# Performance work log

Measured on AMD Instinct MI355X. Metric: run time of the kernel, lower is better.

Reference implementation:

```python
import jax, jax.numpy as jnp
import numpy as np

L = 7
D = 20
V = 2 ** L                      # voxel_size
NUM_EMB = V ** 3
DOM_LO, DOM_HI = -1.0, 1.0
DOM_LEN = DOM_HI - DOM_LO

# 8 corner offsets in the order used by the torch module
OFFSETS = jnp.array([[0, 0, 0], [1, 0, 0], [0, 1, 0], [1, 1, 0],
                     [0, 0, 1], [1, 0, 1], [0, 1, 1], [1, 1, 1]], dtype=jnp.int32)


def setup_inputs() -> dict:
    key = jax.random.key(0)
    kx, kg = jax.random.split(key)
    # points strictly inside the domain so floor()+1 corner stays in-range
    x = jax.random.uniform(kx, (1_000_000, 3), jnp.float32, minval=-1.0, maxval=0.998)
    grid = jax.random.normal(kg, (NUM_EMB, D), jnp.float32) * 0.02  # embedding table
    return {"x": x, "grid": grid}


def reference(x, grid):
    # points -> grid space, floor to lower corner
    gp = jnp.floor((x - DOM_LO) / DOM_LEN * V)                  # [P,3] float
    grid_idx = gp[:, None, :].astype(jnp.int32) + OFFSETS[None]  # [P,8,3]
    # flat index: ix * V^0 + iy * V^1 + iz * V^2
    flat = grid_idx[..., 0] + grid_idx[..., 1] * V + grid_idx[..., 2] * (V * V)
    Q_emb = grid[flat]                                          # [P,8,D] gather
    Q_pos = grid_idx.astype(x.dtype) / V * DOM_LEN + DOM_LO      # [P,8,3] world pos

    px, py, pz = x[:, 0], x[:, 1], x[:, 2]
    x1, x2 = Q_pos[:, 0, 0], Q_pos[:, 1, 0]
    y1, y2 = Q_pos[:, 0, 1], Q_pos[:, 2, 1]
    z1, z2 = Q_pos[:, 0, 2], Q_pos[:, 4, 2]

    q000, q100, q010, q110 = Q_emb[:, 0], Q_emb[:, 1], Q_emb[:, 2], Q_emb[:, 3]
    q001, q101, q011, q111 = Q_emb[:, 4], Q_emb[:, 5], Q_emb[:, 6], Q_emb[:, 7]

    wx0 = ((x2 - px) / (x2 - x1))[:, None]
    wx1 = ((px - x1) / (x2 - x1))[:, None]
    fx0 = wx0 * q000 + wx1 * q100
    fx1 = wx0 * q010 + wx1 * q110
    fx2 = wx0 * q001 + wx1 * q101
    fx3 = wx0 * q011 + wx1 * q111

    wy0 = ((y2 - py) / (y2 - y1))[:, None]
    wy1 = ((py - y1) / (y2 - y1))[:, None]
    fy0 = wy0 * fx0 + wy1 * fx1
    fy1 = wy0 * fx2 + wy1 * fx3

    wz0 = ((z2 - pz) / (z2 - z1))[:, None]
    wz1 = ((pz - z1) / (z2 - z1))[:, None]
    return wz0 * fy0 + wz1 * fy1                                 # [P,D]
```

## Files before the change

### kernel.cpp

```cpp
#include <hip/hip_runtime.h>

#define V 128
#define D 20
#define NUM_EMB (V * V * V)
#define NBUCK 32768
#define BCAP  60
#define OVFCAP 16384
#define REG_ROWS 125
#define REG_CHUNKS 625
#define STAGE_INSTS 10

typedef float v4f __attribute__((ext_vector_type(4)));
typedef unsigned int u32;

typedef const __attribute__((address_space(1))) void gv_t;
typedef __attribute__((address_space(3))) void lv_t;
#define G2L(gsrc, ldst) \
    __builtin_amdgcn_global_load_lds((gv_t*)(gsrc), (lv_t*)(ldst), 16, 0, 0)

__device__ __forceinline__ void compute_chunk(
    const float* __restrict__ x, const float* __restrict__ grid,
    float* __restrict__ out, int i, int k)
{
    float px = x[3 * i + 0];
    float py = x[3 * i + 1];
    float pz = x[3 * i + 2];
    int ix = (int)floorf((px + 1.0f) * 64.0f);
    int iy = (int)floorf((py + 1.0f) * 64.0f);
    int iz = (int)floorf((pz + 1.0f) * 64.0f);

    float x1 = (float)ix * (2.0f / 128.0f) - 1.0f;
    float x2 = (float)(ix + 1) * (2.0f / 128.0f) - 1.0f;
    float y1 = (float)iy * (2.0f / 128.0f) - 1.0f;
    float y2 = (float)(iy + 1) * (2.0f / 128.0f) - 1.0f;
    float z1 = (float)iz * (2.0f / 128.0f) - 1.0f;
    float z2 = (float)(iz + 1) * (2.0f / 128.0f) - 1.0f;

    float wx1 = (px - x1) * 64.0f, wx0 = (x2 - px) * 64.0f;
    float wy1 = (py - y1) * 64.0f, wy0 = (y2 - py) * 64.0f;
    float wz1 = (pz - z1) * 64.0f, wz0 = (z2 - pz) * 64.0f;

    int f000 = ix + iy * V + iz * V * V;
    int flats[8] = { f000,             f000 + 1,
                     f000 + V,         f000 + V + 1,
                     f000 + V * V,     f000 + V * V + 1,
                     f000 + V * V + V, f000 + V * V + V + 1 };
    #pragma unroll
    for (int c = 0; c < 8; c++)
        if (flats[c] > NUM_EMB - 1) flats[c] = NUM_EMB - 1;

    float w[8];
    w[0] = wx0 * wy0 * wz0; w[1] = wx1 * wy0 * wz0;
    w[2] = wx0 * wy1 * wz0; w[3] = wx1 * wy1 * wz0;
    w[4] = wx0 * wy0 * wz1; w[5] = wx1 * wy0 * wz1;
    w[6] = wx0 * wy1 * wz1; w[7] = wx1 * wy1 * wz1;

    v4f q[8];
    #pragma unroll
    for (int c = 0; c < 8; c++)
        q[c] = *(const v4f*)(grid + (size_t)flats[c] * D + 4 * k);

    v4f acc = (v4f)(0.0f);
    #pragma unroll
    for (int c = 0; c < 8; c++) acc += w[c] * q[c];

    __builtin_nontemporal_store(acc, (v4f*)(out + (size_t)i * D + 4 * k));
}

__global__ __launch_bounds__(256) void bin_kernel(
    const float* __restrict__ x, const float* __restrict__ grid,
    float* __restrict__ out, u32* __restrict__ cnt, u32* __restrict__ blist,
    u32* __restrict__ ovfc, u32* __restrict__ ovf, int N)
{
    int i = blockIdx.x * 256 + threadIdx.x;
    if (i >= N) return;
    float px = x[3 * i + 0];
    float py = x[3 * i + 1];
    float pz = x[3 * i + 2];
    int ix = (int)floorf((px + 1.0f) * 64.0f);
    int iy = (int)floorf((py + 1.0f) * 64.0f);
    int iz = (int)floorf((pz + 1.0f) * 64.0f);
    int b = (ix >> 2) + ((iy >> 2) << 5) + ((iz >> 2) << 10);
    u32 pos = atomicAdd(&cnt[b], 1u);
    if (pos < BCAP) {
        blist[(size_t)b * BCAP + pos] = (u32)i;
    } else {
        u32 op = atomicAdd(ovfc, 1u);
        if (op < OVFCAP) ovf[op] = (u32)i;
        else for (int k = 0; k < 5; k++) compute_chunk(x, grid, out, i, k);
    }
}

__global__ __launch_bounds__(128) void gather_kernel(
    const float* __restrict__ x, const float* __restrict__ grid,
    float* __restrict__ out, const u32* __restrict__ cnt,
    const u32* __restrict__ blist)
{
    __shared__ __align__(16) float reg[STAGE_INSTS * 256];

    int bid = blockIdx.x;
    int b = (bid & 7) * (NBUCK / 8) + (bid >> 3);
    int bx = b & 31, by = (b >> 5) & 31, bz = b >> 10;
    int gx0 = bx * 4, gy0 = by * 4, gz0 = bz * 4;

    int tid = threadIdx.x, wave = tid >> 6, lane = tid & 63;

    for (int w = wave; w < STAGE_INSTS; w += 2) {
        int t = w * 64 + lane;
        if (t > REG_CHUNKS - 1) t = REG_CHUNKS - 1;
        int row = t / 5;
        int c   = t - row * 5;
        int sx = row % 5;
        int r5 = row / 5;
        int sy = r5 % 5;
        int sz = r5 / 5;
        int flat = (gx0 + sx) + (gy0 + sy) * V + (gz0 + sz) * (V * V);
        if (flat > NUM_EMB - 1) flat = NUM_EMB - 1;
        G2L(grid + (size_t)flat * D + c * 4, reg + w * 256);
    }

    __syncthreads();

    u32 n = cnt[b];
    if (n > BCAP) n = BCAP;
    int total = (int)n * 5;
    for (int u = tid; u < total; u += 128) {
        int p = u / 5;
        int k = u - p * 5;
        int i = (int)blist[(size_t)b * BCAP + p];
        float px = x[3 * i + 0];
        float py = x[3 * i + 1];
        float pz = x[3 * i + 2];
        float gxf = (px + 1.0f) * 64.0f;
        float gyf = (py + 1.0f) * 64.0f;
        float gzf = (pz + 1.0f) * 64.0f;
        float ixf = floorf(gxf), iyf = floorf(gyf), izf = floorf(gzf);
        float fx = gxf - ixf;
        float fy = gyf - iyf;
        float fz = gzf - izf;
        int lx = (int)ixf - gx0;
        int ly = (int)iyf - gy0;
        int lz = (int)izf - gz0;
        int l000 = (lz * 5 + ly) * 5 + lx;

        v4f acc = (v4f)(0.0f);
        #pragma unroll
        for (int c = 0; c < 8; c++) {
            int l = l000 + (c & 1) + ((c >> 1) & 1) * 5 + ((c >> 2) & 1) * 25;
            v4f q = *(const v4f*)(reg + l * 20 + k * 4);
            float wgt = ((c & 1)        ? fx : 1.0f - fx)
                      * (((c >> 1) & 1) ? fy : 1.0f - fy)
                      * (((c >> 2) & 1) ? fz : 1.0f - fz);
            acc += wgt * q;
        }
        __builtin_nontemporal_store(acc, (v4f*)(out + (size_t)i * D + k * 4));
    }
}

__global__ __launch_bounds__(256) void ovf_kernel(
    const float* __restrict__ x, const float* __restrict__ grid,
    float* __restrict__ out, const u32* __restrict__ ovfc,
    const u32* __restrict__ ovf)
{
    u32 n = *ovfc;
    if (n > OVFCAP) n = OVFCAP;
    int total = (int)n * 5;
    for (int u = blockIdx.x * 256 + threadIdx.x; u < total;
         u += 256 * (int)gridDim.x) {
        int p = u / 5;
        int k = u - p * 5;
        compute_chunk(x, grid, out, (int)ovf[p], k);
    }
}

__global__ __launch_bounds__(320) void naive_kernel(
    const float* __restrict__ x, const float* __restrict__ grid,
    float* __restrict__ out, int N)
{
    int tid = threadIdx.x;
    int lp  = tid / 5;
    int k   = tid - lp * 5;
    int i   = blockIdx.x * 64 + lp;
    if (i >= N) return;
    compute_chunk(x, grid, out, i, k);
}

extern "C" void kernel_launch(void* const* d_in, const int* in_sizes, int n_in,
                              void* d_out, int out_size, void* d_ws, size_t ws_size,
                              hipStream_t stream) {
    const float* x = (const float*)d_in[0];
    const float* grid = (const float*)d_in[1];
    float* out = (float*)d_out;
    int N = in_sizes[0] / 3;

    size_t need = ((size_t)NBUCK + 1 + OVFCAP + (size_t)NBUCK * BCAP) * 4;
    if (d_ws == nullptr || ws_size < need) {
        int nblocks = (N + 63) / 64;
        naive_kernel<<<nblocks, 320, 0, stream>>>(x, grid, out, N);
        return;
    }

    u32* cnt   = (u32*)d_ws;
    u32* ovfc  = cnt + NBUCK;
    u32* ovf   = ovfc + 1;
    u32* blist = ovf + OVFCAP;

    hipMemsetAsync(cnt, 0, (size_t)(NBUCK + 1) * 4, stream);
    bin_kernel<<<(N + 255) / 256, 256, 0, stream>>>(
        x, grid, out, cnt, blist, ovfc, ovf, N);
    gather_kernel<<<NBUCK, 128, 0, stream>>>(x, grid, out, cnt, blist);
    ovf_kernel<<<16, 256, 0, stream>>>(x, grid, out, ovfc, ovf);
}
```

Baseline: 388.5 us.

## Make gather blocks persistent over 16 buckets with double-buffered LDS slab prefetch

Each gather block is now a single wave that walks 16 consecutive buckets instead of handling one. It double-buffers the 5x5x5 grid slab in LDS and prefetches the next bucket's slab through global_load_lds, with explicit waitcnt, while it computes the current bucket. Bucket capacity drops from 60 to 38 and the overflow buffer and its kernel grid grow. The goal is to hide slab load latency and cut per-block launch and sync overhead. The trade-offs are more points routed to the slower overflow path and much less block-level parallelism.

```diff
diff --git a/kernel.cpp b/kernel.cpp
--- a/kernel.cpp
+++ b/kernel.cpp
@@ -4,11 +4,11 @@
 #define D 20
 #define NUM_EMB (V * V * V)
 #define NBUCK 32768
-#define BCAP  60
-#define OVFCAP 16384
-#define REG_ROWS 125
-#define REG_CHUNKS 625
-#define STAGE_INSTS 10
+#define BCAP  38
+#define OVFCAP 32768
+#define NBLK  2048
+#define BPB   (NBUCK / NBLK)
+#define SLABF 2560
 
 typedef float v4f __attribute__((ext_vector_type(4)));
 typedef unsigned int u32;
@@ -91,69 +91,118 @@
     }
 }
 
-__global__ __launch_bounds__(128) void gather_kernel(
+__device__ __forceinline__ void emit_point(
+    const float* slab, int gx0, int gy0, int gz0,
+    float px, float py, float pz, int i, int k, float* __restrict__ out)
+{
+    float gxf = (px + 1.0f) * 64.0f;
+    float gyf = (py + 1.0f) * 64.0f;
+    float gzf = (pz + 1.0f) * 64.0f;
+    float ixf = floorf(gxf), iyf = floorf(gyf), izf = floorf(gzf);
+    float fx = gxf - ixf;
+    float fy = gyf - iyf;
+    float fz = gzf - izf;
+    int lx = (int)ixf - gx0;
+    int ly = (int)iyf - gy0;
+    int lz = (int)izf - gz0;
+    int l000 = (lz * 5 + ly) * 5 + lx;
+
+    v4f acc = (v4f)(0.0f);
+    #pragma unroll
+    for (int c = 0; c < 8; c++) {
+        int l = l000 + (c & 1) + ((c >> 1) & 1) * 5 + ((c >> 2) & 1) * 25;
+        v4f q = *(const v4f*)(slab + l * 20 + k * 4);
+        float wgt = ((c & 1)        ? fx : 1.0f - fx)
+                  * (((c >> 1) & 1) ? fy : 1.0f - fy)
+                  * (((c >> 2) & 1) ? fz : 1.0f - fz);
+        acc += wgt * q;
+    }
+    __builtin_nontemporal_store(acc, (v4f*)(out + (size_t)i * D + k * 4));
+}
+
+__global__ __launch_bounds__(64) void gather_kernel(
     const float* __restrict__ x, const float* __restrict__ grid,
     float* __restrict__ out, const u32* __restrict__ cnt,
     const u32* __restrict__ blist)
 {
-    __shared__ __align__(16) float reg[STAGE_INSTS * 256];
-
-    int bid = blockIdx.x;
-    int b = (bid & 7) * (NBUCK / 8) + (bid >> 3);
-    int bx = b & 31, by = (b >> 5) & 31, bz = b >> 10;
-    int gx0 = bx * 4, gy0 = by * 4, gz0 = bz * 4;
-
-    int tid = threadIdx.x, wave = tid >> 6, lane = tid & 63;
-
-    for (int w = wave; w < STAGE_INSTS; w += 2) {
+    __shared__ __align__(16) float reg[2][SLABF];
+
+    const int lane = threadIdx.x;
+    int j  = blockIdx.x;
+    int jp = (j & 7) * (NBLK / 8) + (j >> 3);
+    const int b0 = jp * BPB;
+
+    int rel[10], cb[10];
+    #pragma unroll
+    for (int w = 0; w < 10; ++w) {
         int t = w * 64 + lane;
-        if (t > REG_CHUNKS - 1) t = REG_CHUNKS - 1;
+        if (t > 624) t = 624;
         int row = t / 5;
         int c   = t - row * 5;
         int sx = row % 5;
         int r5 = row / 5;
         int sy = r5 % 5;
         int sz = r5 / 5;
-        int flat = (gx0 + sx) + (gy0 + sy) * V + (gz0 + sz) * (V * V);
-        if (flat > NUM_EMB - 1) flat = NUM_EMB - 1;
-        G2L(grid + (size_t)flat * D + c * 4, reg + w * 256);
-    }
-
-    __syncthreads();
-
-    u32 n = cnt[b];
-    if (n > BCAP) n = BCAP;
-    int total = (int)n * 5;
-    for (int u = tid; u < total; u += 128) {
-        int p = u / 5;
-        int k = u - p * 5;
-        int i = (int)blist[(size_t)b * BCAP + p];
-        float px = x[3 * i + 0];
-        float py = x[3 * i + 1];
-        float pz = x[3 * i + 2];
-        float gxf = (px + 1.0f) * 64.0f;
-        float gyf = (py + 1.0f) * 64.0f;
-        float gzf = (pz + 1.0f) * 64.0f;
-        float ixf = floorf(gxf), iyf = floorf(gyf), izf = floorf(gzf);
-        float fx = gxf - ixf;
-        float fy = gyf - iyf;
-        float fz = gzf - izf;
-        int lx = (int)ixf - gx0;
-        int ly = (int)iyf - gy0;
-        int lz = (int)izf - gz0;
-        int l000 = (lz * 5 + ly) * 5 + lx;
-
-        v4f acc = (v4f)(0.0f);
+        rel[w] = sx + sy * V + sz * (V * V);
+        cb[w]  = c * 16;
+    }
+    const int p0 = lane / 5,         k0 = lane - 5 * p0;
+    const int p1 = (lane + 64) / 5,  k1 = (lane + 64) - 5 * p1;
+    const int p2 = (lane + 128) / 5, k2 = (lane + 128) - 5 * p2;
+
+    {
+        int b = b0;
+        int fb = ((b & 31) << 2) + (((b >> 5) & 31) << 2) * V
+               + ((b >> 10) << 2) * (V * V);
         #pragma unroll
-        for (int c = 0; c < 8; c++) {
-            int l = l000 + (c & 1) + ((c >> 1) & 1) * 5 + ((c >> 2) & 1) * 25;
-            v4f q = *(const v4f*)(reg + l * 20 + k * 4);
-            float wgt = ((c & 1)        ? fx : 1.0f - fx)
-                      * (((c >> 1) & 1) ? fy : 1.0f - fy)
-                      * (((c >> 2) & 1) ? fz : 1.0f - fz);
-            acc += wgt * q;
+        for (int w = 0; w < 10; ++w) {
+            int flat = fb + rel[w];
+            if (flat > NUM_EMB - 1) flat = NUM_EMB - 1;
+            G2L((const char*)grid + (size_t)flat * 80 + cb[w],
+                &reg[0][0] + w * 256);
         }
-        __builtin_nontemporal_store(acc, (v4f*)(out + (size_t)i * D + k * 4));
+    }
+
+    for (int t = 0; t < BPB; ++t) {
+        const float* cur = &reg[0][0] + ((t & 1) ? SLABF : 0);
+        float*       nxt = &reg[0][0] + ((t & 1) ? 0 : SLABF);
+
+        int b = b0 + t;
+        int gx0 = (b & 31) << 2, gy0 = ((b >> 5) & 31) << 2, gz0 = (b >> 10) << 2;
+
+        u32 n = cnt[b]; if (n > BCAP) n = BCAP;
+        int total = (int)n * 5;
+        bool v0 = lane < total, v1 = lane + 64 < total, v2 = lane + 128 < total;
+        int i0 = 0, i1 = 0, i2 = 0;
+        float px0 = 0, py0 = 0, pz0 = 0, px1 = 0, py1 = 0, pz1 = 0,
+              px2 = 0, py2 = 0, pz2 = 0;
+        if (v0) { i0 = (int)blist[(size_t)b * BCAP + p0];
+                  px0 = x[3*i0]; py0 = x[3*i0+1]; pz0 = x[3*i0+2]; }
+        if (v1) { i1 = (int)blist[(size_t)b * BCAP + p1];
+                  px1 = x[3*i1]; py1 = x[3*i1+1]; pz1 = x[3*i1+2]; }
+        if (v2) { i2 = (int)blist[(size_t)b * BCAP + p2];
+                  px2 = x[3*i2]; py2 = x[3*i2+1]; pz2 = x[3*i2+2]; }
+        __builtin_amdgcn_sched_barrier(0);
+
+        if (t + 1 < BPB) {
+            int bn = b + 1;
+            int fb = ((bn & 31) << 2) + (((bn >> 5) & 31) << 2) * V
+                   + ((bn >> 10) << 2) * (V * V);
+            #pragma unroll
+            for (int w = 0; w < 10; ++w) {
+                int flat = fb + rel[w];
+                if (flat > NUM_EMB - 1) flat = NUM_EMB - 1;
+                G2L((const char*)grid + (size_t)flat * 80 + cb[w], nxt + w * 256);
+            }
+            __builtin_amdgcn_s_waitcnt(0x0F7A);
+        } else {
+            __builtin_amdgcn_s_waitcnt(0x0F70);
+        }
+        __builtin_amdgcn_sched_barrier(0);
+
+        if (v0) emit_point(cur, gx0, gy0, gz0, px0, py0, pz0, i0, k0, out);
+        if (v1) emit_point(cur, gx0, gy0, gz0, px1, py1, pz1, i1, k1, out);
+        if (v2) emit_point(cur, gx0, gy0, gz0, px2, py2, pz2, i2, k2, out);
     }
 }
 
@@ -208,6 +257,6 @@
     hipMemsetAsync(cnt, 0, (size_t)(NBUCK + 1) * 4, stream);
     bin_kernel<<<(N + 255) / 256, 256, 0, stream>>>(
         x, grid, out, cnt, blist, ovfc, ovf, N);
-    gather_kernel<<<NBUCK, 128, 0, stream>>>(x, grid, out, cnt, blist);
-    ovf_kernel<<<16, 256, 0, stream>>>(x, grid, out, ovfc, ovf);
-}
+    gather_kernel<<<NBLK, 64, 0, stream>>>(x, grid, out, cnt, blist);
+    ovf_kernel<<<64, 256, 0, stream>>>(x, grid, out, ovfc, ovf);
+}
```

Measured after the change: 418.4 us. +7.7%, slower.
